# Kernel optimization log

Measured on AMD Instinct MI355X. Metric: run time of the kernel, lower is better.

The kernel has to match this reference:

```python
import jax, jax.numpy as jnp
import numpy as np

L, M, N = 28, 28, 28   # lateral slices, rows, cols (fixed by the tNN module)
BATCH = 65536


def setup_inputs() -> dict:
    key = jax.random.key(0)
    k1, k2, k3 = jax.random.split(key, 3)
    x = jax.random.normal(k1, (L, N, BATCH), dtype=jnp.float32)
    W = jax.random.normal(k2, (L, M, N), dtype=jnp.float32)
    B = jax.random.normal(k3, (L, M, 1), dtype=jnp.float32)
    return {"x": x, "W": W, "B": B}


def t_product(A, X):
    """t-product: out[k] = sum_j A[(k-j) mod l] @ X[j].
    Equivalent to fold(bcirc(A) @ unfold(X)) as in torch_tensor_product,
    but exploits the circulant structure instead of materializing the
    (l*m, l*n) block-circulant matrix."""
    l = A.shape[0]
    idx = (jnp.arange(l)[:, None] - jnp.arange(l)[None, :]) % l  # [k, j]
    Ar = A[idx]  # (l, l, m, n) -- small: l^2 * m * n elements
    return jnp.einsum('kjmn,jnp->kmp', Ar, X)  # (l, m, p)


def reference(x, W, B):
    # forward: relu(W * x + B) with * the tensor t-product
    return jax.nn.relu(t_product(W, x) + B)
```

## Files before the change

kernel.cpp:

```cpp
#include <hip/hip_runtime.h>


typedef __attribute__((ext_vector_type(4))) float f32x4;
typedef __attribute__((ext_vector_type(8))) short s16x8;
typedef __attribute__((ext_vector_type(4))) unsigned int u32x4;

#define BATCH    65536
#define MROWS    784
#define KDIM     784
#define KSTEPS   25
#define BM       112
#define BN       256
#define MT       7
#define NT       256
#define NWG      (MT*NT)
#define ATILE_ELEMS 3584
#define AWS_ELEMS  (MT*KSTEPS*ATILE_ELEMS)

__device__ __forceinline__ unsigned int rne1(float f) {
  unsigned int u = __float_as_uint(f);
  return (u + 0x7fffu + ((u >> 16) & 1u)) >> 16;
}

__device__ __forceinline__ unsigned int cvtpk(float lo, float hi) {
  unsigned int r;
  asm("v_cvt_pk_bf16_f32 %0, %1, %2" : "=v"(r) : "v"(lo), "v"(hi));
  return r;
}

__device__ __forceinline__ int swz(int slot) {
  return (slot * 16) ^ (((slot >> 3) & 7) << 4);
}

typedef const __attribute__((address_space(1))) unsigned int glb_uint;
typedef __attribute__((address_space(3))) unsigned int lds_uint;
__device__ __forceinline__ void async16(const void* g, void* l) {
  __builtin_amdgcn_global_load_lds((glb_uint*)g, (lds_uint*)l, 16, 0, 0);
}

__global__ void build_A(const float* __restrict__ W, unsigned short* __restrict__ A_ws) {
  int idx = blockIdx.x * 256 + threadIdx.x;
  if (idx >= AWS_ELEMS) return;
  int tile = idx / ATILE_ELEMS;
  int o    = idx - tile * ATILE_ELEMS;
  int mt   = tile / KSTEPS;
  int ks   = tile - mt * KSTEPS;
  int e    = o & 7;
  int slot = o >> 3;
  int kb   = slot / BM;
  int ml   = slot - kb * BM;
  int r    = mt * BM + ml;
  int c    = ks * 32 + kb * 8 + e;
  float v = 0.0f;
  if (c < KDIM) {
    int kl = r / 28, mm = r - kl * 28;
    int j  = c / 28, n  = c - j * 28;
    int d = kl - j; if (d < 0) d += 28;
    v = W[(d * 28 + mm) * 28 + n];
  }
  A_ws[idx] = (unsigned short)rne1(v);
}

__global__ __launch_bounds__(256, 2) void tnn_fused(
    const float* __restrict__ X, const unsigned short* __restrict__ A_ws,
    const float* __restrict__ Bias, float* __restrict__ C) {
  __shared__ __align__(16) unsigned short a_lds[ATILE_ELEMS];
  __shared__ __align__(16) unsigned short x_lds[8192];

  int bid = blockIdx.x;
  int wg  = (bid & 7) * (NWG / 8) + (bid >> 3);
  int nt  = wg / MT;
  int mt  = wg - nt * MT;

  int tid  = threadIdx.x;
  int lane = tid & 63;
  int wave = tid >> 6;

  f32x4 acc[7][4];
#pragma unroll
  for (int i = 0; i < 7; ++i)
#pragma unroll
    for (int j = 0; j < 4; ++j)
      acc[i][j] = (f32x4){0.f, 0.f, 0.f, 0.f};

  const float* xbase = X + (size_t)(nt * BN) + ((size_t)(wave * 8) << 16) + (lane << 2);
  int wslot0 = wave * 256 + (lane << 2);

  int a_rd    = (((lane >> 4) * BM) + (lane & 15)) * 16;
  int x_slot0 = (lane >> 4) * 256 + wave * 64 + (lane & 15);

  for (int ks = 0; ks < KSTEPS; ++ks) {
    f32x4 v[8];
    int k0 = ks * 32 + wave * 8;
    const float* xs = xbase + ((size_t)ks << 21);
#pragma unroll
    for (int dk = 0; dk < 8; ++dk) {
      if (k0 + dk < KDIM) v[dk] = *(const f32x4*)(xs + ((size_t)dk << 16));
      else                v[dk] = (f32x4){0.f, 0.f, 0.f, 0.f};
    }

    __syncthreads();

    const unsigned short* atile = A_ws + (size_t)(mt * KSTEPS + ks) * ATILE_ELEMS;
    async16(atile + wave * 512 + lane * 8, &a_lds[wave * 512]);
    if (wave < 3)
      async16(atile + (wave + 4) * 512 + lane * 8, &a_lds[(wave + 4) * 512]);

#pragma unroll
    for (int di = 0; di < 4; ++di) {
      u32x4 w;
      w.x = cvtpk(v[0][di], v[1][di]);
      w.y = cvtpk(v[2][di], v[3][di]);
      w.z = cvtpk(v[4][di], v[5][di]);
      w.w = cvtpk(v[6][di], v[7][di]);
      *(u32x4*)((char*)x_lds + swz(wslot0 + di)) = w;
    }

    __syncthreads();

    s16x8 af[7], xf[4];
#pragma unroll
    for (int i = 0; i < 7; ++i)
      af[i] = *(const s16x8*)((const char*)a_lds + a_rd + i * 256);
#pragma unroll
    for (int jn = 0; jn < 4; ++jn)
      xf[jn] = *(const s16x8*)((const char*)x_lds + swz(x_slot0 + jn * 16));
#pragma unroll
    for (int i = 0; i < 7; ++i)
#pragma unroll
      for (int jn = 0; jn < 4; ++jn)
        acc[i][jn] = __builtin_amdgcn_mfma_f32_16x16x32_bf16(af[i], xf[jn], acc[i][jn], 0, 0, 0);
  }

  int colbase = nt * BN + wave * 64 + (lane & 15);
#pragma unroll
  for (int i = 0; i < 7; ++i) {
    int r0 = mt * BM + i * 16 + ((lane >> 4) << 2);
    f32x4 bv = *(const f32x4*)&Bias[r0];
#pragma unroll
    for (int jn = 0; jn < 4; ++jn) {
      size_t cb = ((size_t)r0 << 16) + (size_t)(colbase + jn * 16);
#pragma unroll
      for (int d = 0; d < 4; ++d) {
        float vv = acc[i][jn][d] + bv[d];
        C[cb + ((size_t)d << 16)] = fmaxf(vv, 0.0f);
      }
    }
  }
}

extern "C" void kernel_launch(void* const* d_in, const int* in_sizes, int n_in,
                              void* d_out, int out_size, void* d_ws, size_t ws_size,
                              hipStream_t stream) {
  const float* x  = (const float*)d_in[0];
  const float* W  = (const float*)d_in[1];
  const float* B  = (const float*)d_in[2];
  float* out = (float*)d_out;
  unsigned short* A_ws = (unsigned short*)d_ws;

  build_A<<<(AWS_ELEMS + 255) / 256, 256, 0, stream>>>(W, A_ws);
  tnn_fused<<<NWG, 256, 0, stream>>>(x, A_ws, B, out);
}
```

Before: 451.7 us.

## Double-buffer A and X LDS tiles to overlap next-step loads with MFMA

Doubles the LDS buffers for the A and X tiles and restructures the K loop into a prologue plus a software pipeline. Each iteration issues the global loads and async LDS copies for the next step, runs the MFMAs on the current buffer, then converts and stores the prefetched X into the other buffer. This hides global load latency behind compute and removes one barrier per step. The cost is double the LDS use and more live registers, which may pressure the two-blocks-per-CU occupancy target.

```diff
diff --git a/kernel.cpp b/kernel.cpp
--- a/kernel.cpp
+++ b/kernel.cpp
@@ -64,8 +64,8 @@
 __global__ __launch_bounds__(256, 2) void tnn_fused(
     const float* __restrict__ X, const unsigned short* __restrict__ A_ws,
     const float* __restrict__ Bias, float* __restrict__ C) {
-  __shared__ __align__(16) unsigned short a_lds[ATILE_ELEMS];
-  __shared__ __align__(16) unsigned short x_lds[8192];
+  __shared__ __align__(16) unsigned short a_lds[2][ATILE_ELEMS];
+  __shared__ __align__(16) unsigned short x_lds[2][8192];
 
   int bid = blockIdx.x;
   int wg  = (bid & 7) * (NWG / 8) + (bid >> 3);
@@ -89,23 +89,18 @@
   int a_rd    = (((lane >> 4) * BM) + (lane & 15)) * 16;
   int x_slot0 = (lane >> 4) * 256 + wave * 64 + (lane & 15);
 
-  for (int ks = 0; ks < KSTEPS; ++ks) {
+  const unsigned short* abase = A_ws + (size_t)mt * KSTEPS * ATILE_ELEMS;
+  int a_st = wave * 512 + lane * 8;
+  int a_ld = wave * 512;
+
+  {
     f32x4 v[8];
-    int k0 = ks * 32 + wave * 8;
-    const float* xs = xbase + ((size_t)ks << 21);
+    const float* xs = xbase;
 #pragma unroll
-    for (int dk = 0; dk < 8; ++dk) {
-      if (k0 + dk < KDIM) v[dk] = *(const f32x4*)(xs + ((size_t)dk << 16));
-      else                v[dk] = (f32x4){0.f, 0.f, 0.f, 0.f};
-    }
-
-    __syncthreads();
-
-    const unsigned short* atile = A_ws + (size_t)(mt * KSTEPS + ks) * ATILE_ELEMS;
-    async16(atile + wave * 512 + lane * 8, &a_lds[wave * 512]);
-    if (wave < 3)
-      async16(atile + (wave + 4) * 512 + lane * 8, &a_lds[(wave + 4) * 512]);
-
+    for (int dk = 0; dk < 8; ++dk) v[dk] = *(const f32x4*)(xs + ((size_t)dk << 16));
+    const unsigned short* at = abase;
+    async16(at + a_st, &a_lds[0][a_ld]);
+    if (wave < 3) async16(at + a_st + 2048, &a_lds[0][a_ld + 2048]);
 #pragma unroll
     for (int di = 0; di < 4; ++di) {
       u32x4 w;
@@ -113,23 +108,60 @@
       w.y = cvtpk(v[2][di], v[3][di]);
       w.z = cvtpk(v[4][di], v[5][di]);
       w.w = cvtpk(v[6][di], v[7][di]);
-      *(u32x4*)((char*)x_lds + swz(wslot0 + di)) = w;
+      *(u32x4*)((char*)x_lds[0] + swz(wslot0 + di)) = w;
     }
+  }
+  __syncthreads();
 
-    __syncthreads();
+  for (int ks = 0; ks < KSTEPS; ++ks) {
+    int cur = ks & 1;
+    bool more = (ks + 1 < KSTEPS);
+
+    f32x4 v[8];
+    if (more) {
+      int ksn = ks + 1;
+      int k0n = ksn * 32 + wave * 8;
+      const float* xs = xbase + ((size_t)ksn << 21);
+      if (k0n + 7 < KDIM) {
+#pragma unroll
+        for (int dk = 0; dk < 8; ++dk) v[dk] = *(const f32x4*)(xs + ((size_t)dk << 16));
+      } else {
+#pragma unroll
+        for (int dk = 0; dk < 8; ++dk)
+          v[dk] = (k0n + dk < KDIM) ? *(const f32x4*)(xs + ((size_t)dk << 16))
+                                    : (f32x4){0.f, 0.f, 0.f, 0.f};
+      }
+      const unsigned short* at = abase + (ks + 1) * ATILE_ELEMS;
+      async16(at + a_st, &a_lds[cur ^ 1][a_ld]);
+      if (wave < 3) async16(at + a_st + 2048, &a_lds[cur ^ 1][a_ld + 2048]);
+    }
 
     s16x8 af[7], xf[4];
 #pragma unroll
     for (int i = 0; i < 7; ++i)
-      af[i] = *(const s16x8*)((const char*)a_lds + a_rd + i * 256);
+      af[i] = *(const s16x8*)((const char*)a_lds[cur] + a_rd + i * 256);
 #pragma unroll
     for (int jn = 0; jn < 4; ++jn)
-      xf[jn] = *(const s16x8*)((const char*)x_lds + swz(x_slot0 + jn * 16));
+      xf[jn] = *(const s16x8*)((const char*)x_lds[cur] + swz(x_slot0 + jn * 16));
 #pragma unroll
     for (int i = 0; i < 7; ++i)
 #pragma unroll
       for (int jn = 0; jn < 4; ++jn)
         acc[i][jn] = __builtin_amdgcn_mfma_f32_16x16x32_bf16(af[i], xf[jn], acc[i][jn], 0, 0, 0);
+
+    if (more) {
+#pragma unroll
+      for (int di = 0; di < 4; ++di) {
+        u32x4 w;
+        w.x = cvtpk(v[0][di], v[1][di]);
+        w.y = cvtpk(v[2][di], v[3][di]);
+        w.z = cvtpk(v[4][di], v[5][di]);
+        w.w = cvtpk(v[6][di], v[7][di]);
+        *(u32x4*)((char*)x_lds[cur ^ 1] + swz(wslot0 + di)) = w;
+      }
+    }
+
+    __syncthreads();
   }
 
   int colbase = nt * BN + wave * 64 + (lane & 15);
```

Result: no change. 451.4 us (-0.1%).
